# Optimization experiments

Measured on AMD Instinct MI355X. Metric: run time of the kernel, lower is better.

The kernel has to match this reference:

```python
import jax, jax.numpy as jnp
import numpy as np

N, H, E, ATTR = 50000, 256, 800000, 107


def _ln(x, g, b, eps=1e-5):
    mu = jnp.mean(x, axis=-1, keepdims=True)
    v = jnp.mean((x - mu) ** 2, axis=-1, keepdims=True)
    return (x - mu) * jax.lax.rsqrt(v + eps) * g + b


def _gcn(x, src, dst, ew, W, b, n):
    # PyG GCNConv with edge_weight: add self-loops (weight 1), symmetric norm
    loop = jnp.arange(n)
    src = jnp.concatenate([src, loop])
    dst = jnp.concatenate([dst, loop])
    ew = jnp.concatenate([ew, jnp.ones((n,), ew.dtype)])
    deg = jax.ops.segment_sum(ew, dst, num_segments=n)  # [n]
    dinv = jnp.where(deg > 0, jax.lax.rsqrt(deg), 0.0)
    norm = dinv[src] * ew * dinv[dst]  # [E+n]
    h = x @ W.T  # [n,H] linear transform first
    agg = jax.ops.segment_sum(norm[:, None] * h[src], dst, num_segments=n)
    return agg + b


def setup_inputs() -> dict:
    key = jax.random.key(0)
    ks = jax.random.split(key, 12)
    s = 1.0 / np.sqrt(H)
    return {
        "x_struct": jax.random.normal(ks[0], (N, H), jnp.float32),
        "edge_index_bold": jax.random.randint(ks[1], (2, E), 0, N),
        "edge_attr_bold": jax.random.uniform(ks[2], (E,), jnp.float32),  # positive weights
        "edge_index_temp": jax.random.randint(ks[3], (2, E), 0, N),
        "edge_attr_temp": jax.random.uniform(ks[4], (E, ATTR), jnp.float32),
        "Wb": jax.random.normal(ks[5], (H, H), jnp.float32) * s,
        "bb": jnp.zeros((H,), jnp.float32),
        "Wt": jax.random.normal(ks[6], (H, H), jnp.float32) * s,
        "bt": jnp.zeros((H,), jnp.float32),
        "W1": jax.random.normal(ks[7], (H, ATTR), jnp.float32) * (1.0 / np.sqrt(ATTR)),
        "b1": jnp.zeros((H,), jnp.float32),
        "g1": jnp.ones((H,), jnp.float32),
        "be1": jnp.zeros((H,), jnp.float32),
        "W2": jax.random.normal(ks[8], (1, H), jnp.float32) * 0.01,
        "b2": jnp.ones((1,), jnp.float32),  # keep temporal edge weights positive
        "gs": jnp.ones((H,), jnp.float32),
        "bs": jnp.zeros((H,), jnp.float32),
        "gt": jnp.ones((H,), jnp.float32),
        "btn": jnp.zeros((H,), jnp.float32),
    }


def reference(x_struct, edge_attr_bold, edge_attr_temp, Wb, bb, Wt, bt,
              W1, b1, g1, be1, W2, b2, gs, bs, gt, btn,
              edge_index_bold, edge_index_temp):
    x = x_struct
    orig = x
    # BOLD-correlation GCN stage: gcn -> residual -> LN -> ReLU
    out = _gcn(x, edge_index_bold[0], edge_index_bold[1], edge_attr_bold, Wb, bb, N)
    x = jax.nn.relu(_ln(out + x, gs, bs))
    # temporal edge-weight MLP: Linear(107->H) -> LN -> ReLU -> Linear(H->1) -> squeeze
    h = jax.nn.relu(_ln(edge_attr_temp @ W1.T + b1, g1, be1))
    w = (h @ W2.T + b2)[:, 0]  # [E]
    # temporal GCN stage: gcn -> residual -> LN -> ReLU
    out = _gcn(x, edge_index_temp[0], edge_index_temp[1], w, Wt, bt, N)
    x = jax.nn.relu(_ln(out + x, gt, btn))
    # final residual with original input through struct_norm
    return _ln(x + orig, gs, bs)
```

## Files before the change

### kernel.cpp

```cpp
#include <hip/hip_runtime.h>

#define HDIM 256
#define KA 107
#define KAP 128

typedef short bf16x8 __attribute__((ext_vector_type(8)));
typedef float f32x4 __attribute__((ext_vector_type(4)));
typedef unsigned short ushort_t;

__device__ inline unsigned short f2bf(float f) {
    union { float f; unsigned u; } v; v.f = f;
    unsigned r = v.u + 0x7fff + ((v.u >> 16) & 1);
    return (unsigned short)(r >> 16);
}

__device__ inline unsigned cvt_pk_bf16(float a, float b) {
    unsigned r;
    asm("v_cvt_pk_bf16_f32 %0, %1, %2" : "=v"(r) : "v"(a), "v"(b));
    return r;
}

__device__ inline float bf_lo(unsigned u) { union { unsigned v; float f; } x; x.v = u << 16; return x.f; }
__device__ inline float bf_hi(unsigned u) { union { unsigned v; float f; } x; x.v = u & 0xffff0000u; return x.f; }

__device__ inline float4 guarded_load4(const float* p, size_t off, size_t tot) {
    if (off + 4 <= tot) return *(const float4*)(p + off);
    float4 r = {0.f, 0.f, 0.f, 0.f};
    float* rr = (float*)&r;
    for (int e = 0; e < 4; ++e) if (off + e < tot) rr[e] = p[off + e];
    return r;
}


__global__ void hist_cnt_kernel(const int* __restrict__ dst, int* cnt, int ne) {
    int e = blockIdx.x * 256 + threadIdx.x;
    if (e < ne) atomicAdd(&cnt[dst[e]], 1);
}

__global__ void f32_to_bf16_kernel(const float* __restrict__ in, ushort_t* __restrict__ out, int n4) {
    int i = blockIdx.x * 256 + threadIdx.x;
    if (i < n4) {
        float4 v = ((const float4*)in)[i];
        uint2 o;
        o.x = cvt_pk_bf16(v.x, v.y);
        o.y = cvt_pk_bf16(v.z, v.w);
        ((uint2*)out)[i] = o;
    }
}

__global__ void prep_all_w_kernel(const float* __restrict__ W1, ushort_t* __restrict__ W1p,
                                  const float* __restrict__ Wb, ushort_t* __restrict__ Wbp,
                                  const float* __restrict__ Wt, ushort_t* __restrict__ Wtp) {
    const int n1 = 256 * KAP, n2 = 256 * 256;
    int i = blockIdx.x * 256 + threadIdx.x;
    if (i < n1) {
        int n = i >> 7, k = i & (KAP - 1);
        W1p[i] = (k < KA) ? f2bf(W1[n * KA + k]) : (ushort_t)0;
    } else if (i < n1 + n2) {
        int j = i - n1;
        Wbp[j] = f2bf(Wb[j]);
    } else if (i < n1 + 2 * n2) {
        int j = i - n1 - n2;
        Wtp[j] = f2bf(Wt[j]);
    }
}

__global__ __launch_bounds__(256) void scan_a_kernel(const int* __restrict__ cnt,
                                                     int* __restrict__ bsum, int n) {
    const int tid = threadIdx.x;
    const int i = blockIdx.x * 256 + tid;
    int v = (i < n) ? cnt[i] : 0;
    int s = v;
#pragma unroll
    for (int d = 1; d < 64; d <<= 1) s += __shfl_xor(s, d);
    __shared__ int ws[4];
    if ((tid & 63) == 0) ws[tid >> 6] = s;
    __syncthreads();
    if (tid == 0) bsum[blockIdx.x] = ws[0] + ws[1] + ws[2] + ws[3];
}

__global__ __launch_bounds__(256) void scan_b_kernel(int* __restrict__ bsum, int nb) {
    const int tid = threadIdx.x;
    int v = (tid < nb) ? bsum[tid] : 0;
    const int lane = tid & 63, wid = tid >> 6;
    int incl = v;
#pragma unroll
    for (int d = 1; d < 64; d <<= 1) { int m = __shfl_up(incl, d); if (lane >= d) incl += m; }
    __shared__ int ws[4];
    if (lane == 63) ws[wid] = incl;
    __syncthreads();
    if (tid < 4) {
        int wv = ws[tid];
        int iv = wv;
#pragma unroll
        for (int d = 1; d < 4; d <<= 1) { int m = __shfl_up(iv, d, 4); if (tid >= d) iv += m; }
        ws[tid] = iv - wv;
    }
    __syncthreads();
    if (tid < nb) bsum[tid] = (incl - v) + ws[wid];
}

__global__ __launch_bounds__(256) void scan_c_kernel(const int* __restrict__ cnt,
                                                     const int* __restrict__ bsum,
                                                     int* __restrict__ rptr,
                                                     int* __restrict__ cur, int n) {
    const int tid = threadIdx.x;
    const int i = blockIdx.x * 256 + tid;
    int v = (i < n) ? cnt[i] : 0;
    const int lane = tid & 63, wid = tid >> 6;
    int incl = v;
#pragma unroll
    for (int d = 1; d < 64; d <<= 1) { int m = __shfl_up(incl, d); if (lane >= d) incl += m; }
    __shared__ int ws[4];
    if (lane == 63) ws[wid] = incl;
    __syncthreads();
    if (tid < 4) {
        int wv = ws[tid];
        int iv = wv;
#pragma unroll
        for (int d = 1; d < 4; d <<= 1) { int m = __shfl_up(iv, d, 4); if (tid >= d) iv += m; }
        ws[tid] = iv - wv;
    }
    __syncthreads();
    const int excl = (incl - v) + ws[wid] + bsum[blockIdx.x];
    if (i < n) { rptr[i] = excl; cur[i] = excl; }
    if (i == n - 1) rptr[n] = excl + v;
}

__global__ void fill_kernel(const int* __restrict__ src, const int* __restrict__ dst,
                            const float* __restrict__ w,
                            int* cur, uint2* __restrict__ edata, int ne) {
    int e = blockIdx.x * 256 + threadIdx.x;
    if (e < ne) {
        int d = dst[e];
        int pos = atomicAdd(&cur[d], 1);
        uint2 ed;
        ed.x = (unsigned)src[e];
        ed.y = __float_as_uint(w[e]);
        edata[pos] = ed;
    }
}

__global__ void deg_kernel(const uint2* __restrict__ edata, const int* __restrict__ rptr,
                           float* __restrict__ dinv, int n) {
    int v = blockIdx.x * 256 + threadIdx.x;
    if (v < n) {
        const int b = rptr[v], e = rptr[v + 1];
        float s = 1.0f;
        for (int i = b; i < e; ++i) s += __uint_as_float(edata[i].y);
        dinv[v] = s > 0.f ? rsqrtf(s) : 0.f;
    }
}

__global__ __launch_bounds__(256) void agg_kernel(const ushort_t* __restrict__ Xb,
                                                  const int* __restrict__ rptr,
                                                  const uint2* __restrict__ edata,
                                                  const float* __restrict__ dinv,
                                                  ushort_t* __restrict__ out, int n) {
    const int v = blockIdx.x * 4 + (threadIdx.x >> 6);
    if (v >= n) return;
    const int lane = threadIdx.x & 63;
    const float dv = dinv[v];
    const uint2 xv = *(const uint2*)(Xb + (size_t)v * HDIM + lane * 4);
    const float dv2 = dv * dv;
    float a0[8], a1[8], a2[8], a3[8];
#pragma unroll
    for (int c = 0; c < 8; ++c) { a0[c] = 0.f; a1[c] = 0.f; a2[c] = 0.f; a3[c] = 0.f; }
    a0[0] = dv2 * bf_lo(xv.x); a1[0] = dv2 * bf_hi(xv.x);
    a2[0] = dv2 * bf_lo(xv.y); a3[0] = dv2 * bf_hi(xv.y);

    const int b = rptr[v];
    const int total = rptr[v + 1] - b;
    uint2 pv[8]; float pn[8];
#pragma unroll
    for (int c = 0; c < 8; ++c) {
        if (c < total) {
            uint2 ed = edata[b + c];
            pn[c] = dinv[ed.x] * __uint_as_float(ed.y) * dv;
            pv[c] = *(const uint2*)(Xb + (size_t)ed.x * HDIM + lane * 4);
        }
    }
    for (int base = 0; base < total; base += 8) {
#pragma unroll
        for (int c = 0; c < 8; ++c) {
            if (base + c < total) {
                uint2 cv = pv[c]; float cn = pn[c];
                int nx = base + 8 + c;
                if (nx < total) {
                    uint2 ed = edata[b + nx];
                    pn[c] = dinv[ed.x] * __uint_as_float(ed.y) * dv;
                    pv[c] = *(const uint2*)(Xb + (size_t)ed.x * HDIM + lane * 4);
                }
                a0[c] = fmaf(cn, bf_lo(cv.x), a0[c]);
                a1[c] = fmaf(cn, bf_hi(cv.x), a1[c]);
                a2[c] = fmaf(cn, bf_lo(cv.y), a2[c]);
                a3[c] = fmaf(cn, bf_hi(cv.y), a3[c]);
            }
        }
    }
    float r0 = ((a0[0] + a0[1]) + (a0[2] + a0[3])) + ((a0[4] + a0[5]) + (a0[6] + a0[7]));
    float r1 = ((a1[0] + a1[1]) + (a1[2] + a1[3])) + ((a1[4] + a1[5]) + (a1[6] + a1[7]));
    float r2 = ((a2[0] + a2[1]) + (a2[2] + a2[3])) + ((a2[4] + a2[5]) + (a2[6] + a2[7]));
    float r3 = ((a3[0] + a3[1]) + (a3[2] + a3[3])) + ((a3[4] + a3[5]) + (a3[6] + a3[7]));
    uint2 o;
    o.x = cvt_pk_bf16(r0, r1);
    o.y = cvt_pk_bf16(r2, r3);
    *(uint2*)(out + (size_t)v * HDIM + lane * 4) = o;
}

__global__ __launch_bounds__(256) void mlp_mfma_kernel(
    const float* __restrict__ A,
    const ushort_t* __restrict__ Wp,
    const float* __restrict__ b1v, const float* __restrict__ g1v,
    const float* __restrict__ be1v, const float* __restrict__ W2,
    const float* __restrict__ b2s, float* __restrict__ out,
    int M, int ntiles) {
    __shared__ ushort_t As[2][64][136];
    __shared__ float ps1[64][4], ps2[64][4], pd[64][4];
    const int tid = threadIdx.x;
    const int l = tid & 63, wv = tid >> 6, g = l >> 4, c = l & 15;
    const float b2sc = b2s[0];
    const size_t tot = (size_t)M * KA;

    for (int z = tid; z < 2 * 64 * 16; z += 256) {
        int buf = z >> 10;
        int rem = z & 1023;
        As[buf][rem >> 4][112 + (rem & 15)] = 0;
    }

    const ushort_t* wb = Wp + (size_t)(wv * 64 + c) * KAP + g * 8;
    bf16x8 wreg[4][2];
#pragma unroll
    for (int ks = 0; ks < 4; ++ks)
#pragma unroll
        for (int nt = 0; nt < 2; ++nt)
            wreg[ks][nt] = *(const bf16x8*)(wb + nt * 16 * KAP + ks * 32);

    const int srow = tid >> 2, sj = tid & 3;
    float4 sreg[7];

    const int t0 = blockIdx.x;
    if (t0 < ntiles) {
        const size_t roff = (size_t)(t0 * 64 + srow) * KA + sj * 4;
#pragma unroll
        for (int i = 0; i < 7; ++i) sreg[i] = guarded_load4(A, roff + i * 16, tot);
#pragma unroll
        for (int i = 0; i < 7; ++i) {
            uint2 o;
            o.x = cvt_pk_bf16(sreg[i].x, sreg[i].y);
            o.y = cvt_pk_bf16(sreg[i].z, sreg[i].w);
            *(uint2*)&As[0][srow][sj * 4 + i * 16] = o;
        }
    }
    __syncthreads();

    int cur = 0;
    for (int t = t0; t < ntiles; t += gridDim.x) {
        const int tn = t + gridDim.x;
        const bool have_next = tn < ntiles;
        if (have_next) {
            const size_t roff = (size_t)(tn * 64 + srow) * KA + sj * 4;
#pragma unroll
            for (int i = 0; i < 7; ++i) sreg[i] = guarded_load4(A, roff + i * 16, tot);
        }

        f32x4 acc[4][4];
#pragma unroll
        for (int rt = 0; rt < 4; ++rt)
#pragma unroll
            for (int nt = 0; nt < 4; ++nt) acc[rt][nt] = (f32x4){0.f, 0.f, 0.f, 0.f};
        __builtin_amdgcn_s_setprio(1);
#pragma unroll
        for (int ks = 0; ks < 4; ++ks) {
            bf16x8 af[4];
#pragma unroll
            for (int rt = 0; rt < 4; ++rt)
                af[rt] = *(const bf16x8*)&As[cur][rt * 16 + c][ks * 32 + g * 8];
#pragma unroll
            for (int nt = 0; nt < 4; ++nt) {
                bf16x8 wfr = (nt < 2) ? wreg[ks][nt]
                                      : *(const bf16x8*)(wb + nt * 16 * KAP + ks * 32);
#pragma unroll
                for (int rt = 0; rt < 4; ++rt)
                    acc[rt][nt] = __builtin_amdgcn_mfma_f32_16x16x32_bf16(wfr, af[rt], acc[rt][nt], 0, 0, 0);
            }
        }
        __builtin_amdgcn_s_setprio(0);

        const int nb = wv * 64 + (g << 2);
        const int m0 = t * 64;
#pragma unroll
        for (int rt = 0; rt < 4; ++rt) {
            float s1 = 0.f, s2 = 0.f;
#pragma unroll
            for (int nt = 0; nt < 4; ++nt) {
                const float4 b4 = *(const float4*)(b1v + nb + nt * 16);
                f32x4 v = acc[rt][nt];
                v[0] += b4.x; v[1] += b4.y; v[2] += b4.z; v[3] += b4.w;
                acc[rt][nt] = v;
                s1 += v[0] + v[1] + v[2] + v[3];
                s2 += v[0] * v[0] + v[1] * v[1] + v[2] * v[2] + v[3] * v[3];
            }
            s1 += __shfl_xor(s1, 16); s1 += __shfl_xor(s1, 32);
            s2 += __shfl_xor(s2, 16); s2 += __shfl_xor(s2, 32);
            if (l < 16) { ps1[rt * 16 + c][wv] = s1; ps2[rt * 16 + c][wv] = s2; }
        }
        __syncthreads();
#pragma unroll
        for (int rt = 0; rt < 4; ++rt) {
            float4 p1 = *(const float4*)ps1[rt * 16 + c];
            float4 p2 = *(const float4*)ps2[rt * 16 + c];
            float s1 = p1.x + p1.y + p1.z + p1.w;
            float s2 = p2.x + p2.y + p2.z + p2.w;
            float mu = s1 * (1.f / HDIM);
            float var = s2 * (1.f / HDIM) - mu * mu;
            float rs = rsqrtf(var + 1e-5f);
            float dacc = 0.f;
#pragma unroll
            for (int nt = 0; nt < 4; ++nt) {
                const float4 g4 = *(const float4*)(g1v + nb + nt * 16);
                const float4 e4 = *(const float4*)(be1v + nb + nt * 16);
                const float4 w4 = *(const float4*)(W2 + nb + nt * 16);
                f32x4 v = acc[rt][nt];
                float y0 = fmaxf((v[0] - mu) * rs * g4.x + e4.x, 0.f);
                float y1 = fmaxf((v[1] - mu) * rs * g4.y + e4.y, 0.f);
                float y2 = fmaxf((v[2] - mu) * rs * g4.z + e4.z, 0.f);
                float y3 = fmaxf((v[3] - mu) * rs * g4.w + e4.w, 0.f);
                dacc = fmaf(y0, w4.x, dacc); dacc = fmaf(y1, w4.y, dacc);
                dacc = fmaf(y2, w4.z, dacc); dacc = fmaf(y3, w4.w, dacc);
            }
            dacc += __shfl_xor(dacc, 16); dacc += __shfl_xor(dacc, 32);
            if (l < 16) pd[rt * 16 + c][wv] = dacc;
        }
        if (have_next) {
#pragma unroll
            for (int i = 0; i < 7; ++i) {
                uint2 o;
                o.x = cvt_pk_bf16(sreg[i].x, sreg[i].y);
                o.y = cvt_pk_bf16(sreg[i].z, sreg[i].w);
                *(uint2*)&As[cur ^ 1][srow][sj * 4 + i * 16] = o;
            }
        }
        __syncthreads();
        if (tid < 64) {
            float4 p = *(const float4*)pd[tid];
            int gr = m0 + tid;
            if (gr < M) out[gr] = p.x + p.y + p.z + p.w + b2sc;
        }
        cur ^= 1;
    }
}

template <int MODE>
__global__ __launch_bounds__(256) void gemm_node_kernel(
    const ushort_t* __restrict__ A,
    const ushort_t* __restrict__ Wp,
    const float* __restrict__ bias,
    const ushort_t* __restrict__ res_bf,
    const ushort_t* __restrict__ orig_bf,
    const float* __restrict__ g1v, const float* __restrict__ b1v,
    const float* __restrict__ g2v, const float* __restrict__ b2v,
    float* __restrict__ out, ushort_t* __restrict__ out_bf, int M) {
    __shared__ ushort_t As[64][264];
    __shared__ float ps1[64][4], ps2[64][4], ps3[64][4], ps4[64][4];
    const int tid = threadIdx.x;
    const int m0 = blockIdx.x * 64;
    const int l = tid & 63, wv = tid >> 6, g = l >> 4, c = l & 15;

    {
        const int r = tid >> 2, j = tid & 3;
        const ushort_t* gsrc = A + (size_t)(m0 + r) * HDIM;
        const bool ok = (m0 + r) < M;
#pragma unroll
        for (int i = 0; i < 8; ++i) {
            const int ci = i * 4 + j;
            bf16x8 v = (bf16x8){0,0,0,0,0,0,0,0};
            if (ok) v = *(const bf16x8*)(gsrc + ci * 8);
            *(bf16x8*)&As[r][ci * 8] = v;
        }
    }
    __syncthreads();

    f32x4 acc[4][4];
#pragma unroll
    for (int rt = 0; rt < 4; ++rt)
#pragma unroll
        for (int nt = 0; nt < 4; ++nt) acc[rt][nt] = (f32x4){0.f, 0.f, 0.f, 0.f};

    const ushort_t* wb = Wp + (size_t)(wv * 64 + c) * HDIM + g * 8;
    __builtin_amdgcn_s_setprio(1);
#pragma unroll
    for (int ks = 0; ks < 8; ++ks) {
        bf16x8 af[4];
#pragma unroll
        for (int rt = 0; rt < 4; ++rt)
            af[rt] = *(const bf16x8*)&As[rt * 16 + c][ks * 32 + g * 8];
#pragma unroll
        for (int nt = 0; nt < 4; ++nt) {
            bf16x8 bfr = *(const bf16x8*)(wb + nt * 16 * HDIM + ks * 32);
#pragma unroll
            for (int rt = 0; rt < 4; ++rt)
                acc[rt][nt] = __builtin_amdgcn_mfma_f32_16x16x32_bf16(bfr, af[rt], acc[rt][nt], 0, 0, 0);
        }
    }
    __builtin_amdgcn_s_setprio(0);

    const int nb = wv * 64 + (g << 2);
#pragma unroll
    for (int rt = 0; rt < 4; ++rt) {
        const int m = m0 + rt * 16 + c;
        const bool vm = m < M;
        const ushort_t* rrow = res_bf + (size_t)m * HDIM + nb;
        float s1 = 0.f, s2 = 0.f;
#pragma unroll
        for (int nt = 0; nt < 4; ++nt) {
            const float4 b4 = *(const float4*)(bias + nb + nt * 16);
            float4 r4 = {0.f, 0.f, 0.f, 0.f};
            if (vm) {
                uint2 rb = *(const uint2*)(rrow + nt * 16);
                r4.x = bf_lo(rb.x); r4.y = bf_hi(rb.x);
                r4.z = bf_lo(rb.y); r4.w = bf_hi(rb.y);
            }
            f32x4 v = acc[rt][nt];
            v[0] += b4.x + r4.x; v[1] += b4.y + r4.y;
            v[2] += b4.z + r4.z; v[3] += b4.w + r4.w;
            acc[rt][nt] = v;
            s1 += v[0] + v[1] + v[2] + v[3];
            s2 += v[0] * v[0] + v[1] * v[1] + v[2] * v[2] + v[3] * v[3];
        }
        s1 += __shfl_xor(s1, 16); s1 += __shfl_xor(s1, 32);
        s2 += __shfl_xor(s2, 16); s2 += __shfl_xor(s2, 32);
        if (l < 16) { ps1[rt * 16 + c][wv] = s1; ps2[rt * 16 + c][wv] = s2; }
    }
    __syncthreads();
#pragma unroll
    for (int rt = 0; rt < 4; ++rt) {
        const int m = m0 + rt * 16 + c;
        const bool vm = m < M;
        float4 p1 = *(const float4*)ps1[rt * 16 + c];
        float4 p2 = *(const float4*)ps2[rt * 16 + c];
        float s1 = p1.x + p1.y + p1.z + p1.w;
        float s2 = p2.x + p2.y + p2.z + p2.w;
        float mu = s1 * (1.f / HDIM);
        float var = s2 * (1.f / HDIM) - mu * mu;
        float rs = rsqrtf(var + 1e-5f);
        if constexpr (MODE == 0) {
            ushort_t* obrow = out_bf + (size_t)m * HDIM + nb;
#pragma unroll
            for (int nt = 0; nt < 4; ++nt) {
                const float4 g4 = *(const float4*)(g1v + nb + nt * 16);
                const float4 e4 = *(const float4*)(b1v + nb + nt * 16);
                f32x4 v = acc[rt][nt];
                float o0 = fmaxf((v[0] - mu) * rs * g4.x + e4.x, 0.f);
                float o1 = fmaxf((v[1] - mu) * rs * g4.y + e4.y, 0.f);
                float o2 = fmaxf((v[2] - mu) * rs * g4.z + e4.z, 0.f);
                float o3 = fmaxf((v[3] - mu) * rs * g4.w + e4.w, 0.f);
                if (vm) {
                    uint2 ob;
                    ob.x = cvt_pk_bf16(o0, o1);
                    ob.y = cvt_pk_bf16(o2, o3);
                    *(uint2*)(obrow + nt * 16) = ob;
                }
            }
        } else {
            const ushort_t* grow = orig_bf + (size_t)m * HDIM + nb;
            float t1 = 0.f, t2 = 0.f;
#pragma unroll
            for (int nt = 0; nt < 4; ++nt) {
                const float4 g4 = *(const float4*)(g1v + nb + nt * 16);
                const float4 e4 = *(const float4*)(b1v + nb + nt * 16);
                float4 o4 = {0.f, 0.f, 0.f, 0.f};
                if (vm) {
                    uint2 gb = *(const uint2*)(grow + nt * 16);
                    o4.x = bf_lo(gb.x); o4.y = bf_hi(gb.x);
                    o4.z = bf_lo(gb.y); o4.w = bf_hi(gb.y);
                }
                f32x4 v = acc[rt][nt];
                f32x4 u;
                u[0] = fmaxf((v[0] - mu) * rs * g4.x + e4.x, 0.f) + o4.x;
                u[1] = fmaxf((v[1] - mu) * rs * g4.y + e4.y, 0.f) + o4.y;
                u[2] = fmaxf((v[2] - mu) * rs * g4.z + e4.z, 0.f) + o4.z;
                u[3] = fmaxf((v[3] - mu) * rs * g4.w + e4.w, 0.f) + o4.w;
                acc[rt][nt] = u;
                t1 += u[0] + u[1] + u[2] + u[3];
                t2 += u[0] * u[0] + u[1] * u[1] + u[2] * u[2] + u[3] * u[3];
            }
            t1 += __shfl_xor(t1, 16); t1 += __shfl_xor(t1, 32);
            t2 += __shfl_xor(t2, 16); t2 += __shfl_xor(t2, 32);
            if (l < 16) { ps3[rt * 16 + c][wv] = t1; ps4[rt * 16 + c][wv] = t2; }
        }
    }
    if constexpr (MODE == 1) {
        __syncthreads();
#pragma unroll
        for (int rt = 0; rt < 4; ++rt) {
            const int m = m0 + rt * 16 + c;
            const bool vm = m < M;
            float4 p1 = *(const float4*)ps3[rt * 16 + c];
            float4 p2 = *(const float4*)ps4[rt * 16 + c];
            float s1 = p1.x + p1.y + p1.z + p1.w;
            float s2 = p2.x + p2.y + p2.z + p2.w;
            float mu2 = s1 * (1.f / HDIM);
            float var2 = s2 * (1.f / HDIM) - mu2 * mu2;
            float rs2 = rsqrtf(var2 + 1e-5f);
            float* orow = out + (size_t)m * HDIM + nb;
#pragma unroll
            for (int nt = 0; nt < 4; ++nt) {
                const float4 g4 = *(const float4*)(g2v + nb + nt * 16);
                const float4 e4 = *(const float4*)(b2v + nb + nt * 16);
                f32x4 u = acc[rt][nt];
                float4 o;
                o.x = (u[0] - mu2) * rs2 * g4.x + e4.x;
                o.y = (u[1] - mu2) * rs2 * g4.y + e4.y;
                o.z = (u[2] - mu2) * rs2 * g4.z + e4.z;
                o.w = (u[3] - mu2) * rs2 * g4.w + e4.w;
                if (vm) *(float4*)(orow + nt * 16) = o;
            }
        }
    }
}


extern "C" void kernel_launch(void* const* d_in, const int* in_sizes, int n_in,
                              void* d_out, int out_size, void* d_ws, size_t ws_size,
                              hipStream_t stream) {
    const float* x    = (const float*)d_in[0];
    const int*   eib  = (const int*)d_in[1];
    const float* eab  = (const float*)d_in[2];
    const int*   eit  = (const int*)d_in[3];
    const float* eat  = (const float*)d_in[4];
    const float* Wb   = (const float*)d_in[5];
    const float* bb   = (const float*)d_in[6];
    const float* Wt   = (const float*)d_in[7];
    const float* bt   = (const float*)d_in[8];
    const float* W1   = (const float*)d_in[9];
    const float* b1   = (const float*)d_in[10];
    const float* g1   = (const float*)d_in[11];
    const float* be1  = (const float*)d_in[12];
    const float* W2   = (const float*)d_in[13];
    const float* b2   = (const float*)d_in[14];
    const float* gs   = (const float*)d_in[15];
    const float* bs   = (const float*)d_in[16];
    const float* gt   = (const float*)d_in[17];
    const float* btn  = (const float*)d_in[18];

    const int Nn = in_sizes[0] / HDIM;
    const int Ne = in_sizes[2];

    const int* src_b = eib;  const int* dst_b = eib + Ne;
    const int* src_t = eit;  const int* dst_t = eit + Ne;

    char* w = (char*)d_ws;
    ushort_t* aggb = (ushort_t*)w; w += (size_t)Nn * HDIM * 2;
    ushort_t* xb   = (ushort_t*)w; w += (size_t)Nn * HDIM * 2;
    ushort_t* x1b  = (ushort_t*)w; w += (size_t)Nn * HDIM * 2;
    float*    wtmp = (float*)w;    w += (size_t)Ne * 4;
    float*    dinv = (float*)w;    w += (size_t)Nn * 4;
    int*      cnt  = (int*)w;      w += (size_t)Nn * 4;
    int*      rptr = (int*)w;      w += (size_t)(Nn + 4) * 4;
    int*      cur  = (int*)w;      w += (size_t)Nn * 4;
    uint2*    edata = (uint2*)w;   w += (size_t)Ne * 8;
    int*      bsum = (int*)w;      w += (size_t)256 * 4;
    ushort_t* W1p  = (ushort_t*)w; w += (size_t)256 * KAP * 2;
    ushort_t* Wbp  = (ushort_t*)w; w += (size_t)256 * 256 * 2;
    ushort_t* Wtp  = (ushort_t*)w; w += (size_t)256 * 256 * 2;

    float* out = (float*)d_out;
    dim3 b256(256);
    dim3 gN((Nn + 255) / 256), gE((Ne + 255) / 256);
    const int nbScan = (Nn + 255) / 256;
    dim3 gAgg((Nn + 3) / 4);
    dim3 gGemmN((Nn + 63) / 64);
    const int ntiles = (Ne + 63) / 64;
    dim3 gMlp(512);
    const int n4 = Nn * HDIM / 4;
    dim3 gCvt((n4 + 255) / 256);
    const int nPrep = 256 * KAP + 2 * 256 * 256;

    prep_all_w_kernel<<<dim3((nPrep + 255) / 256), b256, 0, stream>>>(W1, W1p, Wb, Wbp, Wt, Wtp);
    f32_to_bf16_kernel<<<gCvt, b256, 0, stream>>>(x, xb, n4);

    hipMemsetAsync(cnt, 0, (size_t)Nn * 4, stream);
    hist_cnt_kernel<<<gE, b256, 0, stream>>>(dst_b, cnt, Ne);
    scan_a_kernel<<<dim3(nbScan), b256, 0, stream>>>(cnt, bsum, Nn);
    scan_b_kernel<<<dim3(1), b256, 0, stream>>>(bsum, nbScan);
    scan_c_kernel<<<dim3(nbScan), b256, 0, stream>>>(cnt, bsum, rptr, cur, Nn);
    fill_kernel<<<gE, b256, 0, stream>>>(src_b, dst_b, eab, cur, edata, Ne);
    deg_kernel<<<gN, b256, 0, stream>>>(edata, rptr, dinv, Nn);
    agg_kernel<<<gAgg, b256, 0, stream>>>(xb, rptr, edata, dinv, aggb, Nn);
    gemm_node_kernel<0><<<gGemmN, b256, 0, stream>>>(
        aggb, Wbp, bb, xb, nullptr, gs, bs, nullptr, nullptr, nullptr, x1b, Nn);

    mlp_mfma_kernel<<<gMlp, b256, 0, stream>>>(
        eat, W1p, b1, g1, be1, W2, b2, wtmp, Ne, ntiles);

    hipMemsetAsync(cnt, 0, (size_t)Nn * 4, stream);
    hist_cnt_kernel<<<gE, b256, 0, stream>>>(dst_t, cnt, Ne);
    scan_a_kernel<<<dim3(nbScan), b256, 0, stream>>>(cnt, bsum, Nn);
    scan_b_kernel<<<dim3(1), b256, 0, stream>>>(bsum, nbScan);
    scan_c_kernel<<<dim3(nbScan), b256, 0, stream>>>(cnt, bsum, rptr, cur, Nn);
    fill_kernel<<<gE, b256, 0, stream>>>(src_t, dst_t, wtmp, cur, edata, Ne);
    deg_kernel<<<gN, b256, 0, stream>>>(edata, rptr, dinv, Nn);
    agg_kernel<<<gAgg, b256, 0, stream>>>(x1b, rptr, edata, dinv, aggb, Nn);
    gemm_node_kernel<1><<<gGemmN, b256, 0, stream>>>(
        aggb, Wtp, bt, x1b, xb, gt, btn, gs, bs, out, nullptr, Nn);
}
```

Measured before the change: 775.2 us.

## Split each node's edge aggregation across four wavefronts with shared-memory reduction

```diff
diff --git a/kernel.cpp b/kernel.cpp
--- a/kernel.cpp
+++ b/kernel.cpp
@@ -157,37 +157,46 @@
                                                   const uint2* __restrict__ edata,
                                                   const float* __restrict__ dinv,
                                                   ushort_t* __restrict__ out, int n) {
-    const int v = blockIdx.x * 4 + (threadIdx.x >> 6);
-    if (v >= n) return;
+    __shared__ float4 part[3][64];
+    const int wvq  = threadIdx.x >> 6;
     const int lane = threadIdx.x & 63;
+    const int v = blockIdx.x;
+
     const float dv = dinv[v];
-    const uint2 xv = *(const uint2*)(Xb + (size_t)v * HDIM + lane * 4);
-    const float dv2 = dv * dv;
-    float a0[8], a1[8], a2[8], a3[8];
-#pragma unroll
-    for (int c = 0; c < 8; ++c) { a0[c] = 0.f; a1[c] = 0.f; a2[c] = 0.f; a3[c] = 0.f; }
-    a0[0] = dv2 * bf_lo(xv.x); a1[0] = dv2 * bf_hi(xv.x);
-    a2[0] = dv2 * bf_lo(xv.y); a3[0] = dv2 * bf_hi(xv.y);
-
     const int b = rptr[v];
     const int total = rptr[v + 1] - b;
+    const int per = (total + 3) >> 2;
+    const int s0 = min(wvq * per, total);
+    const int mc = min(per, total - s0);
+    const int mb = b + s0;
+
+    float a0[8], a1[8], a2[8], a3[8];
+#pragma unroll
+    for (int c = 0; c < 8; ++c) { a0[c] = 0.f; a1[c] = 0.f; a2[c] = 0.f; a3[c] = 0.f; }
+    if (wvq == 0) {
+        const uint2 xv = *(const uint2*)(Xb + (size_t)v * HDIM + lane * 4);
+        const float dv2 = dv * dv;
+        a0[0] = dv2 * bf_lo(xv.x); a1[0] = dv2 * bf_hi(xv.x);
+        a2[0] = dv2 * bf_lo(xv.y); a3[0] = dv2 * bf_hi(xv.y);
+    }
+
     uint2 pv[8]; float pn[8];
 #pragma unroll
     for (int c = 0; c < 8; ++c) {
-        if (c < total) {
-            uint2 ed = edata[b + c];
+        if (c < mc) {
+            uint2 ed = edata[mb + c];
             pn[c] = dinv[ed.x] * __uint_as_float(ed.y) * dv;
             pv[c] = *(const uint2*)(Xb + (size_t)ed.x * HDIM + lane * 4);
         }
     }
-    for (int base = 0; base < total; base += 8) {
+    for (int base = 0; base < mc; base += 8) {
 #pragma unroll
         for (int c = 0; c < 8; ++c) {
-            if (base + c < total) {
+            if (base + c < mc) {
                 uint2 cv = pv[c]; float cn = pn[c];
                 int nx = base + 8 + c;
-                if (nx < total) {
-                    uint2 ed = edata[b + nx];
+                if (nx < mc) {
+                    uint2 ed = edata[mb + nx];
                     pn[c] = dinv[ed.x] * __uint_as_float(ed.y) * dv;
                     pv[c] = *(const uint2*)(Xb + (size_t)ed.x * HDIM + lane * 4);
                 }
@@ -202,10 +211,18 @@
     float r1 = ((a1[0] + a1[1]) + (a1[2] + a1[3])) + ((a1[4] + a1[5]) + (a1[6] + a1[7]));
     float r2 = ((a2[0] + a2[1]) + (a2[2] + a2[3])) + ((a2[4] + a2[5]) + (a2[6] + a2[7]));
     float r3 = ((a3[0] + a3[1]) + (a3[2] + a3[3])) + ((a3[4] + a3[5]) + (a3[6] + a3[7]));
-    uint2 o;
-    o.x = cvt_pk_bf16(r0, r1);
-    o.y = cvt_pk_bf16(r2, r3);
-    *(uint2*)(out + (size_t)v * HDIM + lane * 4) = o;
+
+    if (wvq) part[wvq - 1][lane] = (float4){r0, r1, r2, r3};
+    __syncthreads();
+    if (wvq == 0) {
+        const float4 p1 = part[0][lane];
+        const float4 p2 = part[1][lane];
+        const float4 p3 = part[2][lane];
+        uint2 o;
+        o.x = cvt_pk_bf16((r0 + p1.x) + (p2.x + p3.x), (r1 + p1.y) + (p2.y + p3.y));
+        o.y = cvt_pk_bf16((r2 + p1.z) + (p2.z + p3.z), (r3 + p1.w) + (p2.w + p3.w));
+        *(uint2*)(out + (size_t)v * HDIM + lane * 4) = o;
+    }
 }
 
 __global__ __launch_bounds__(256) void mlp_mfma_kernel(
@@ -569,7 +586,7 @@
     dim3 b256(256);
     dim3 gN((Nn + 255) / 256), gE((Ne + 255) / 256);
     const int nbScan = (Nn + 255) / 256;
-    dim3 gAgg((Nn + 3) / 4);
+    dim3 gAgg(Nn);
     dim3 gGemmN((Nn + 63) / 64);
     const int ntiles = (Ne + 63) / 64;
     dim3 gMlp(512);
```

Result: no change. 769.0 us (-0.8%).
